# Optimization experiments

Hardware: AMD Instinct MI355X
Metric: run time of the kernel (lower is better)

Reference implementation:

```python
import jax, jax.numpy as jnp
import numpy as np

VOCAB = 50000
E = 300        # embedding_dim
HID = 512      # hidden_dim (bidirectional total)
HD = HID // 2  # per-direction hidden
K = 20         # tagset size
START = 18
STOP = 19
B = 64
T = 256
NEG = -10000.0


def setup_inputs() -> dict:
    key = jax.random.key(0)
    ks = jax.random.split(key, 12)
    s = 0.1
    sentence = jax.random.randint(ks[0], (B, T), 0, VOCAB)
    length = jax.random.randint(ks[1], (B,), T // 2, T + 1)
    embed_table = jax.random.normal(ks[2], (VOCAB, E)) * s
    w_ih_f = jax.random.normal(ks[3], (4 * HD, E)) * s
    w_hh_f = jax.random.normal(ks[4], (4 * HD, HD)) * s
    b_f = jax.random.normal(ks[5], (4 * HD,)) * s
    w_ih_b = jax.random.normal(ks[6], (4 * HD, E)) * s
    w_hh_b = jax.random.normal(ks[7], (4 * HD, HD)) * s
    b_b = jax.random.normal(ks[8], (4 * HD,)) * s
    W_out = jax.random.normal(ks[9], (K, HID)) * s
    b_out = jax.random.normal(ks[10], (K,)) * s
    transitions = jax.random.normal(ks[11], (K, K))
    transitions = transitions.at[START, :].set(NEG).at[:, STOP].set(NEG)
    return dict(sentence=sentence, length=length, embed_table=embed_table,
                w_ih_f=w_ih_f, w_hh_f=w_hh_f, b_f=b_f,
                w_ih_b=w_ih_b, w_hh_b=w_hh_b, b_b=b_b,
                W_out=W_out, b_out=b_out, transitions=transitions)


def _lstm(xs, w_ih, w_hh, b, reverse):
    # xs: [T, B, E]; PyTorch gate order i, f, g, o
    Bn = xs.shape[1]
    H = w_hh.shape[1]

    def step(carry, x):
        h, c = carry
        g = x @ w_ih.T + h @ w_hh.T + b
        i, f, gg, o = jnp.split(g, 4, axis=-1)
        c = jax.nn.sigmoid(f) * c + jax.nn.sigmoid(i) * jnp.tanh(gg)
        h = jax.nn.sigmoid(o) * jnp.tanh(c)
        return (h, c), h

    init = (jnp.zeros((Bn, H), xs.dtype), jnp.zeros((Bn, H), xs.dtype))
    _, hs = jax.lax.scan(step, init, xs, reverse=reverse)
    return hs  # [T, B, H], time-ordered


def _viterbi(feats, length, transitions):
    # feats: [B, T, K]; vectorized over batch, scan over time
    Bn, Tn, Kn = feats.shape
    fv0 = jnp.full((Bn, Kn), NEG, feats.dtype).at[:, START].set(0.0)
    idk = jnp.arange(Kn)

    def step(fv, inp):
        feat_t, t = inp
        # scores[b, next, prev] = fv[b, prev] + transitions[next, prev]
        sc = fv[:, None, :] + transitions[None, :, :]
        bp = jnp.argmax(sc, axis=-1)              # [B, K]
        best = jnp.max(sc, axis=-1) + feat_t      # [B, K]
        m = (t < length)[:, None]
        fv_new = jnp.where(m, best, fv)           # freeze past sentence end
        bp = jnp.where(m, bp, idk[None, :])       # identity backpointer on pad
        return fv_new, bp

    fv, bps = jax.lax.scan(step, fv0, (jnp.swapaxes(feats, 0, 1), jnp.arange(Tn)))
    term = fv + transitions[STOP][None, :]
    last = jnp.argmax(term, axis=-1)              # [B]
    score = jnp.max(term, axis=-1)                # [B] viterbi max score

    def back(tag, bp_t):
        prev = jnp.take_along_axis(bp_t, tag[:, None], axis=1)[:, 0]
        return prev, tag

    _, path_t = jax.lax.scan(back, last, bps, reverse=True)  # [T, B], time order
    path = jnp.swapaxes(path_t, 0, 1)             # [B, T]; entries >= length repeat last tag
    return score, path


def reference(sentence, length, embed_table, w_ih_f, w_hh_f, b_f,
              w_ih_b, w_hh_b, b_b, W_out, b_out, transitions):
    embeds = embed_table[sentence]                # [B, T, E]
    xs = jnp.swapaxes(embeds, 0, 1)               # [T, B, E]
    hf = _lstm(xs, w_ih_f, w_hh_f, b_f, reverse=False)
    hb = _lstm(xs, w_ih_b, w_hh_b, b_b, reverse=True)
    h = jnp.concatenate([hf, hb], axis=-1)        # [T, B, HID]
    feats = h @ W_out.T + b_out                   # [T, B, K]
    feats = jnp.swapaxes(feats, 0, 1)             # [B, T, K]
    score, path = _viterbi(feats, length, transitions)
    return score, path
```

## Files before the change

### kernel.cpp

```cpp
#include <hip/hip_runtime.h>
#include <hip/hip_bf16.h>

#define DINL __device__ __forceinline__

namespace {

typedef unsigned long long u64;

constexpr int Tn = 256;
constexpr int Bn = 64;
constexpr int HDn = 256;
constexpr int Kt = 20;
constexpr int STOPt = 19;
constexpr int STARTt = 18;
constexpr float NEGV = -10000.0f;

DINL float sigm(float x) { return 1.0f / (1.0f + __expf(-x)); }
DINL float tanh_f(float x) {
  float ax = fabsf(x);
  float e = __expf(-2.0f * ax);
  float t = (1.0f - e) / (1.0f + e);
  return x < 0.0f ? -t : t;
}

__global__ void k_epoch(unsigned* ep) {
  if (threadIdx.x == 0)
    __hip_atomic_fetch_add(ep, 1u, __ATOMIC_RELAXED, __HIP_MEMORY_SCOPE_AGENT);
}

__global__ void k_wt(const float* __restrict__ wf, const float* __restrict__ wb,
                     float* __restrict__ Wt) {
  int idx = blockIdx.x * 256 + threadIdx.x;
  if (idx >= 300 * 2048) return;
  int k = idx >> 11, n = idx & 2047;
  const float* w = (n < 1024) ? wf : wb;
  int nn = n & 1023;
  Wt[idx] = w[nn * 300 + k];
}

__global__ __launch_bounds__(256) void k_xproj(
    const int* __restrict__ sentence, const float* __restrict__ table,
    const float* __restrict__ Wt, const float* __restrict__ b_f,
    const float* __restrict__ b_b, float* __restrict__ xproj) {
  __shared__ float As[20][68];
  __shared__ float Bs[20][136];
  __shared__ int tok[64];

  int tid = threadIdx.x;
  int t = blockIdx.x;
  int n0 = blockIdx.y * 128;

  if (tid < 64) tok[tid] = sentence[tid * Tn + t];
  __syncthreads();

  int ty = tid >> 4, tx = tid & 15;
  float acc[4][8];
#pragma unroll
  for (int i = 0; i < 4; ++i)
#pragma unroll
    for (int j = 0; j < 8; ++j) acc[i][j] = 0.0f;

  for (int k0 = 0; k0 < 300; k0 += 20) {
#pragma unroll
    for (int i = 0; i < 5; ++i) {
      int idx = i * 256 + tid;
      int r = idx / 20, kk = idx % 20;
      As[kk][r] = table[tok[r] * 300 + k0 + kk];
    }
#pragma unroll
    for (int i = 0; i < 10; ++i) {
      int idx = i * 256 + tid;
      int kk = idx >> 7, c = idx & 127;
      Bs[kk][c] = Wt[(k0 + kk) * 2048 + n0 + c];
    }
    __syncthreads();
#pragma unroll
    for (int kk = 0; kk < 20; ++kk) {
      float4 a4 = *(const float4*)&As[kk][ty * 4];
      float4 b4a = *(const float4*)&Bs[kk][tx * 8];
      float4 b4b = *(const float4*)&Bs[kk][tx * 8 + 4];
      float av[4] = {a4.x, a4.y, a4.z, a4.w};
      float bvv[8] = {b4a.x, b4a.y, b4a.z, b4a.w, b4b.x, b4b.y, b4b.z, b4b.w};
#pragma unroll
      for (int i = 0; i < 4; ++i)
#pragma unroll
        for (int j = 0; j < 8; ++j) acc[i][j] += av[i] * bvv[j];
    }
    __syncthreads();
  }

  float bias[8];
#pragma unroll
  for (int j = 0; j < 8; ++j) {
    int n = n0 + tx * 8 + j;
    bias[j] = (n < 1024) ? b_f[n] : b_b[n - 1024];
  }
#pragma unroll
  for (int i = 0; i < 4; ++i) {
    size_t m = (size_t)t * 64 + ty * 4 + i;
    float* dst = &xproj[m * 2048 + n0 + tx * 8];
    float4 v0 = {acc[i][0] + bias[0], acc[i][1] + bias[1], acc[i][2] + bias[2],
                 acc[i][3] + bias[3]};
    float4 v1 = {acc[i][4] + bias[4], acc[i][5] + bias[5], acc[i][6] + bias[6],
                 acc[i][7] + bias[7]};
    *(float4*)dst = v0;
    *(float4*)(dst + 4) = v1;
  }
}

__global__ __launch_bounds__(128) void k_lstm(
    const float* __restrict__ whh_f, const float* __restrict__ whh_b,
    const float* __restrict__ xproj, float* __restrict__ h_all,
    int* __restrict__ flags, int* __restrict__ xcdtab,
    const unsigned* __restrict__ ep) {
  __shared__ __align__(16) float hl[16 * 256];
  __shared__ int fastsh;

  int tid = threadIdx.x;
  int bid = blockIdx.x;
  int gid = bid & 7;
  int s = bid >> 3;
  int dir = gid >> 2;
  int bg = gid & 3;
  const float* whh = dir ? whh_b : whh_f;

  int c = tid >> 4;
  int kc = tid & 15;

  unsigned E =
      __hip_atomic_load(ep, __ATOMIC_RELAXED, __HIP_MEMORY_SCOPE_AGENT);
  unsigned xcd = __builtin_amdgcn_s_getreg((3 << 11) | (0 << 6) | 20) & 0xFu;
  if (tid == 0) {
    __hip_atomic_store(&xcdtab[(gid << 5) + s],
                       (int)((E << 4) | xcd), __ATOMIC_RELAXED,
                       __HIP_MEMORY_SCOPE_AGENT);
  }
  if (tid < 64) {
    const int* xp_ = xcdtab + (gid << 5) + (tid & 31);
    unsigned v;
    for (;;) {
      v = (unsigned)__hip_atomic_load(xp_, __ATOMIC_RELAXED,
                                      __HIP_MEMORY_SCOPE_AGENT);
      bool rdy = (v >> 4) == (E & 0x0FFFFFFFu);
      if (__all((tid < 32) ? rdy : 1)) break;
      __builtin_amdgcn_s_sleep(1);
    }
    int mine = (int)(v & 0xFu);
    int ref = __shfl(mine, 0, 64);
    bool eq = (mine == ref);
    bool alleq = __all((tid < 32) ? eq : 1);
    if (tid == 0) fastsh = alleq ? 1 : 0;
  }

  float4 w4[4][4];
#pragma unroll
  for (int g = 0; g < 4; ++g) {
    const float* src = whh + ((size_t)(g * 256 + s * 8 + c)) * 256;
#pragma unroll
    for (int jj = 0; jj < 4; ++jj)
      w4[g][jj] = *(const float4*)(src + ((kc + (jj << 4)) << 2));
  }

  __syncthreads();
  const bool fast = (fastsh != 0);
  const unsigned base = E * 256u;

  float c_reg = 0.0f;

  for (int st = 0; st < Tn; ++st) {
    int xt = dir ? (Tn - 1 - st) : st;

    float xp[4];
    {
      size_t xb = ((size_t)(xt * 64 + bg * 16 + kc)) * 2048 + dir * 1024 +
                  s * 8 + c;
#pragma unroll
      for (int g = 0; g < 4; ++g) xp[g] = xproj[xb + g * 256];
    }

    float acc[16][4];
#pragma unroll
    for (int b = 0; b < 16; ++b)
#pragma unroll
      for (int g = 0; g < 4; ++g) acc[b][g] = 0.0f;

    if (st > 0) {
      if (tid < 64) {
        const int* fp = flags + ((gid << 5) + (tid & 31)) * 4;
        for (;;) {
          unsigned v = (unsigned)__hip_atomic_load(
              fp, __ATOMIC_RELAXED, __HIP_MEMORY_SCOPE_AGENT);
          int d = (int)(v - base);
          if (__all((tid < 32) ? (d >= st) : 1)) break;
          __builtin_amdgcn_s_sleep(1);
        }
      }
      __syncthreads();

      int pt = dir ? (xt + 1) : (xt - 1);
      const float* hsrc =
          h_all + ((size_t)(dir * Tn + pt) * 64 + bg * 16) * 256;
      const char* tb = (const char*)hsrc + (size_t)tid * 16;
      const char* p0 = tb;
      const char* p1 = tb + 4096;
      const char* p2 = tb + 8192;
      const char* p3 = tb + 12288;
      float4 q0, q1, q2, q3, q4, q5, q6, q7;
      asm volatile(
          "global_load_dwordx4 %0, %8, off sc1\n\t"
          "global_load_dwordx4 %1, %8, off offset:2048 sc1\n\t"
          "global_load_dwordx4 %2, %9, off sc1\n\t"
          "global_load_dwordx4 %3, %9, off offset:2048 sc1\n\t"
          "global_load_dwordx4 %4, %10, off sc1\n\t"
          "global_load_dwordx4 %5, %10, off offset:2048 sc1\n\t"
          "global_load_dwordx4 %6, %11, off sc1\n\t"
          "global_load_dwordx4 %7, %11, off offset:2048 sc1\n\t"
          "s_waitcnt vmcnt(0)"
          : "=&v"(q0), "=&v"(q1), "=&v"(q2), "=&v"(q3), "=&v"(q4), "=&v"(q5),
            "=&v"(q6), "=&v"(q7)
          : "v"(p0), "v"(p1), "v"(p2), "v"(p3));
      *(float4*)&hl[(tid + 0 * 128) << 2] = q0;
      *(float4*)&hl[(tid + 1 * 128) << 2] = q1;
      *(float4*)&hl[(tid + 2 * 128) << 2] = q2;
      *(float4*)&hl[(tid + 3 * 128) << 2] = q3;
      *(float4*)&hl[(tid + 4 * 128) << 2] = q4;
      *(float4*)&hl[(tid + 5 * 128) << 2] = q5;
      *(float4*)&hl[(tid + 6 * 128) << 2] = q6;
      *(float4*)&hl[(tid + 7 * 128) << 2] = q7;
      __syncthreads();

#pragma unroll
      for (int b = 0; b < 16; ++b) {
#pragma unroll
        for (int jj = 0; jj < 4; ++jj) {
          float4 hv = *(const float4*)&hl[b * 256 + ((kc + (jj << 4)) << 2)];
#pragma unroll
          for (int g = 0; g < 4; ++g) {
            acc[b][g] += w4[g][jj].x * hv.x + w4[g][jj].y * hv.y +
                         w4[g][jj].z * hv.z + w4[g][jj].w * hv.w;
          }
        }
      }
    }

#pragma unroll
    for (int r = 0; r < 4; ++r) {
      int m = 1 << r;
      int kb = (kc >> r) & 1;
#pragma unroll
      for (int ii = 0; ii < (16 >> (r + 1)); ++ii) {
#pragma unroll
        for (int g = 0; g < 4; ++g) {
          float e = acc[2 * ii][g], o = acc[2 * ii + 1][g];
          float kept = kb ? o : e;
          float sent = kb ? e : o;
          acc[ii][g] = kept + __shfl_xor(sent, m, 64);
        }
      }
    }

    {
      float gi = acc[0][0] + xp[0];
      float gf = acc[0][1] + xp[1];
      float gg = acc[0][2] + xp[2];
      float go = acc[0][3] + xp[3];
      c_reg = sigm(gf) * c_reg + sigm(gi) * tanh_f(gg);
      float h = sigm(go) * tanh_f(c_reg);
      size_t hi = ((size_t)(dir * Tn + xt) * 64 + bg * 16 + kc) * 256 + s * 8 +
                  c;
      if (fast) {
        h_all[hi] = h;
      } else {
        __hip_atomic_store(&h_all[hi], h, __ATOMIC_RELAXED,
                           __HIP_MEMORY_SCOPE_AGENT);
      }
    }

    asm volatile("s_waitcnt vmcnt(0)" ::: "memory");
    __syncthreads();
    if (tid == 0) {
      int fv = (int)(base + (unsigned)(st + 1));
      if (fast) {
        flags[((gid << 5) + s) * 4] = fv;
      } else {
        __hip_atomic_store(flags + ((gid << 5) + s) * 4, fv, __ATOMIC_RELAXED,
                           __HIP_MEMORY_SCOPE_AGENT);
      }
    }
  }
}

__global__ __launch_bounds__(256) void k_feats(const float* __restrict__ h_all,
                                               const float* __restrict__ Wout,
                                               const float* __restrict__ bout,
                                               float* __restrict__ feats) {
  __shared__ float Wl[20 * 512];
  __shared__ float hlf[64 * 256];

  int tid = threadIdx.x;
  int t = blockIdx.x;
  for (int i = tid; i < 20 * 512; i += 256) Wl[i] = Wout[i];

  float acc[5] = {0, 0, 0, 0, 0};
  int b = tid & 63, kg5 = tid >> 6;
  int swz = b & 7;

  for (int d = 0; d < 2; ++d) {
    __syncthreads();
    const float* hsrc = h_all + ((size_t)(d * Tn + t)) * 64 * 256;
#pragma unroll 8
    for (int i = 0; i < 64; ++i) {
      int idx = i * 256 + tid;
      int hb = idx >> 8, k = idx & 255;
      hlf[hb * 256 + 4 * ((k >> 2) ^ (hb & 7)) + (k & 3)] = hsrc[idx];
    }
    __syncthreads();
    for (int jg = 0; jg < 64; ++jg) {
      float4 hv = *(const float4*)&hlf[b * 256 + 4 * (jg ^ swz)];
#pragma unroll
      for (int kk = 0; kk < 5; ++kk) {
        int krow = kg5 * 5 + kk;
        float4 wvv = *(const float4*)&Wl[krow * 512 + d * 256 + jg * 4];
        acc[kk] += hv.x * wvv.x + hv.y * wvv.y + hv.z * wvv.z + hv.w * wvv.w;
      }
    }
  }
#pragma unroll
  for (int kk = 0; kk < 5; ++kk) {
    int krow = kg5 * 5 + kk;
    feats[((size_t)b * Tn + t) * Kt + krow] = acc[kk] + bout[krow];
  }
}

__global__ __launch_bounds__(64) void k_viterbi(const float* __restrict__ feats,
                                                const float* __restrict__ trans,
                                                const int* __restrict__ length,
                                                float* __restrict__ out) {
  __shared__ float tr[400];
  __shared__ float fv[20];
  __shared__ float term[20];
  __shared__ unsigned char bps[256][20];

  int b = blockIdx.x;
  int lane = threadIdx.x;
  for (int i = lane; i < 400; i += 64) tr[i] = trans[i];
  if (lane < 20) fv[lane] = (lane == STARTt) ? 0.0f : NEGV;
  int len = length[b];
  __syncthreads();

  for (int t = 0; t < Tn; ++t) {
    float nf = 0.0f;
    int bp = 0;
    if (lane < 20) {
      if (t < len) {
        float vmax = -3.4e38f;
        int pb = 0;
#pragma unroll
        for (int p = 0; p < 20; ++p) {
          float v = fv[p] + tr[lane * 20 + p];
          if (v > vmax) { vmax = v; pb = p; }
        }
        nf = vmax + feats[((size_t)b * Tn + t) * Kt + lane];
        bp = pb;
      } else {
        nf = fv[lane];
        bp = lane;
      }
    }
    __syncthreads();
    if (lane < 20) {
      fv[lane] = nf;
      bps[t][lane] = (unsigned char)bp;
    }
    __syncthreads();
  }

  if (lane < 20) term[lane] = fv[lane] + tr[STOPt * 20 + lane];
  __syncthreads();
  if (lane == 0) {
    float smax = term[0];
    int last = 0;
    for (int p = 1; p < 20; ++p)
      if (term[p] > smax) { smax = term[p]; last = p; }
    out[b] = smax;
    int tag = last;
    for (int t = Tn - 1; t >= 0; --t) {
      out[64 + b * Tn + t] = (float)tag;
      tag = bps[t][tag];
    }
  }
}

}

extern "C" void kernel_launch(void* const* d_in, const int* in_sizes, int n_in,
                              void* d_out, int out_size, void* d_ws,
                              size_t ws_size, hipStream_t stream) {
  const int* sentence = (const int*)d_in[0];
  const int* length = (const int*)d_in[1];
  const float* table = (const float*)d_in[2];
  const float* w_ih_f = (const float*)d_in[3];
  const float* w_hh_f = (const float*)d_in[4];
  const float* b_f = (const float*)d_in[5];
  const float* w_ih_b = (const float*)d_in[6];
  const float* w_hh_b = (const float*)d_in[7];
  const float* b_b = (const float*)d_in[8];
  const float* W_out = (const float*)d_in[9];
  const float* b_out = (const float*)d_in[10];
  const float* trans = (const float*)d_in[11];
  float* out = (float*)d_out;

  float* ws = (float*)d_ws;
  float* xproj = ws;
  float* h_all = ws + (size_t)33554432;
  float* Wt = h_all + (size_t)8388608;
  float* feats = Wt + (size_t)300 * 2048;
  int* flags = (int*)(feats + (size_t)Bn * Tn * Kt);
  int* xcdtab = flags + 1024;
  unsigned* ep = (unsigned*)(xcdtab + 256);
  (void)ws_size; (void)in_sizes; (void)n_in; (void)out_size;

  k_epoch<<<dim3(1), dim3(64), 0, stream>>>(ep);
  k_wt<<<dim3(2400), dim3(256), 0, stream>>>(w_ih_f, w_ih_b, Wt);
  k_xproj<<<dim3(256, 16), dim3(256), 0, stream>>>(sentence, table, Wt, b_f,
                                                   b_b, xproj);
  k_lstm<<<dim3(256), dim3(128), 0, stream>>>(w_hh_f, w_hh_b, xproj, h_all,
                                              flags, xcdtab, ep);
  k_feats<<<dim3(256), dim3(256), 0, stream>>>(h_all, W_out, b_out, feats);
  k_viterbi<<<dim3(64), dim3(64), 0, stream>>>(feats, trans, length, out);
}
```

Baseline: 1.480 ms.

## Replace LSTM per-step flag barrier with epoch-tagged hidden-state words

Each hidden value is now stored as a 64-bit word that packs the float with an epoch-and-step tag. Consumers check these tags directly instead of polling a separate per-block flag array after a store-drain and block barrier, which takes the flag round-trip and the producer-side waitcnt/syncthreads off the sequential recurrence. The cost is twice the bytes per hidden-state read and write, plus a retry loop that re-reads the whole batch when tags are stale. The xproj loads also become nontemporal.

```diff
diff --git a/kernel.cpp b/kernel.cpp
--- a/kernel.cpp
+++ b/kernel.cpp
@@ -21,6 +21,10 @@
   float e = __expf(-2.0f * ax);
   float t = (1.0f - e) / (1.0f + e);
   return x < 0.0f ? -t : t;
+}
+
+DINL void agent_st64(u64* p, u64 v) {
+  __hip_atomic_store(p, v, __ATOMIC_RELAXED, __HIP_MEMORY_SCOPE_AGENT);
 }
 
 __global__ void k_epoch(unsigned* ep) {
@@ -110,9 +114,8 @@
 
 __global__ __launch_bounds__(128) void k_lstm(
     const float* __restrict__ whh_f, const float* __restrict__ whh_b,
-    const float* __restrict__ xproj, float* __restrict__ h_all,
-    int* __restrict__ flags, int* __restrict__ xcdtab,
-    const unsigned* __restrict__ ep) {
+    const float* __restrict__ xproj, u64* __restrict__ h_ep,
+    int* __restrict__ xcdtab, const unsigned* __restrict__ ep) {
   __shared__ __align__(16) float hl[16 * 256];
   __shared__ int fastsh;
 
@@ -131,9 +134,8 @@
       __hip_atomic_load(ep, __ATOMIC_RELAXED, __HIP_MEMORY_SCOPE_AGENT);
   unsigned xcd = __builtin_amdgcn_s_getreg((3 << 11) | (0 << 6) | 20) & 0xFu;
   if (tid == 0) {
-    __hip_atomic_store(&xcdtab[(gid << 5) + s],
-                       (int)((E << 4) | xcd), __ATOMIC_RELAXED,
-                       __HIP_MEMORY_SCOPE_AGENT);
+    __hip_atomic_store(&xcdtab[(gid << 5) + s], (int)((E << 4) | xcd),
+                       __ATOMIC_RELAXED, __HIP_MEMORY_SCOPE_AGENT);
   }
   if (tid < 64) {
     const int* xp_ = xcdtab + (gid << 5) + (tid & 31);
@@ -163,7 +165,7 @@
 
   __syncthreads();
   const bool fast = (fastsh != 0);
-  const unsigned base = E * 256u;
+  const unsigned base = E * 512u;
 
   float c_reg = 0.0f;
 
@@ -175,7 +177,8 @@
       size_t xb = ((size_t)(xt * 64 + bg * 16 + kc)) * 2048 + dir * 1024 +
                   s * 8 + c;
 #pragma unroll
-      for (int g = 0; g < 4; ++g) xp[g] = xproj[xb + g * 256];
+      for (int g = 0; g < 4; ++g)
+        xp[g] = __builtin_nontemporal_load(&xproj[xb + g * 256]);
     }
 
     float acc[16][4];
@@ -185,48 +188,83 @@
       for (int g = 0; g < 4; ++g) acc[b][g] = 0.0f;
 
     if (st > 0) {
-      if (tid < 64) {
-        const int* fp = flags + ((gid << 5) + (tid & 31)) * 4;
-        for (;;) {
-          unsigned v = (unsigned)__hip_atomic_load(
-              fp, __ATOMIC_RELAXED, __HIP_MEMORY_SCOPE_AGENT);
-          int d = (int)(v - base);
-          if (__all((tid < 32) ? (d >= st) : 1)) break;
-          __builtin_amdgcn_s_sleep(1);
-        }
-      }
-      __syncthreads();
-
       int pt = dir ? (xt + 1) : (xt - 1);
-      const float* hsrc =
-          h_all + ((size_t)(dir * Tn + pt) * 64 + bg * 16) * 256;
+      const u64* hsrc =
+          h_ep + ((size_t)(dir * Tn + pt) * 64 + bg * 16) * 256;
       const char* tb = (const char*)hsrc + (size_t)tid * 16;
       const char* p0 = tb;
       const char* p1 = tb + 4096;
       const char* p2 = tb + 8192;
       const char* p3 = tb + 12288;
-      float4 q0, q1, q2, q3, q4, q5, q6, q7;
-      asm volatile(
-          "global_load_dwordx4 %0, %8, off sc1\n\t"
-          "global_load_dwordx4 %1, %8, off offset:2048 sc1\n\t"
-          "global_load_dwordx4 %2, %9, off sc1\n\t"
-          "global_load_dwordx4 %3, %9, off offset:2048 sc1\n\t"
-          "global_load_dwordx4 %4, %10, off sc1\n\t"
-          "global_load_dwordx4 %5, %10, off offset:2048 sc1\n\t"
-          "global_load_dwordx4 %6, %11, off sc1\n\t"
-          "global_load_dwordx4 %7, %11, off offset:2048 sc1\n\t"
-          "s_waitcnt vmcnt(0)"
-          : "=&v"(q0), "=&v"(q1), "=&v"(q2), "=&v"(q3), "=&v"(q4), "=&v"(q5),
-            "=&v"(q6), "=&v"(q7)
-          : "v"(p0), "v"(p1), "v"(p2), "v"(p3));
-      *(float4*)&hl[(tid + 0 * 128) << 2] = q0;
-      *(float4*)&hl[(tid + 1 * 128) << 2] = q1;
-      *(float4*)&hl[(tid + 2 * 128) << 2] = q2;
-      *(float4*)&hl[(tid + 3 * 128) << 2] = q3;
-      *(float4*)&hl[(tid + 4 * 128) << 2] = q4;
-      *(float4*)&hl[(tid + 5 * 128) << 2] = q5;
-      *(float4*)&hl[(tid + 6 * 128) << 2] = q6;
-      *(float4*)&hl[(tid + 7 * 128) << 2] = q7;
+      const char* p4 = tb + 16384;
+      const char* p5 = tb + 20480;
+      const char* p6 = tb + 24576;
+      const char* p7 = tb + 28672;
+      uint4 q0, q1, q2, q3, q4, q5, q6, q7;
+      uint4 q8, q9, q10, q11, q12, q13, q14, q15;
+      unsigned tgt = base + (unsigned)st;
+#define BATCH_READ()                                                        \
+  asm volatile(                                                             \
+      "global_load_dwordx4 %0, %16, off sc1\n\t"                            \
+      "global_load_dwordx4 %1, %16, off offset:2048 sc1\n\t"                \
+      "global_load_dwordx4 %2, %17, off sc1\n\t"                            \
+      "global_load_dwordx4 %3, %17, off offset:2048 sc1\n\t"                \
+      "global_load_dwordx4 %4, %18, off sc1\n\t"                            \
+      "global_load_dwordx4 %5, %18, off offset:2048 sc1\n\t"                \
+      "global_load_dwordx4 %6, %19, off sc1\n\t"                            \
+      "global_load_dwordx4 %7, %19, off offset:2048 sc1\n\t"                \
+      "global_load_dwordx4 %8, %20, off sc1\n\t"                            \
+      "global_load_dwordx4 %9, %20, off offset:2048 sc1\n\t"                \
+      "global_load_dwordx4 %10, %21, off sc1\n\t"                           \
+      "global_load_dwordx4 %11, %21, off offset:2048 sc1\n\t"               \
+      "global_load_dwordx4 %12, %22, off sc1\n\t"                           \
+      "global_load_dwordx4 %13, %22, off offset:2048 sc1\n\t"               \
+      "global_load_dwordx4 %14, %23, off sc1\n\t"                           \
+      "global_load_dwordx4 %15, %23, off offset:2048 sc1\n\t"               \
+      "s_waitcnt vmcnt(0)"                                                  \
+      : "=&v"(q0), "=&v"(q1), "=&v"(q2), "=&v"(q3), "=&v"(q4), "=&v"(q5),   \
+        "=&v"(q6), "=&v"(q7), "=&v"(q8), "=&v"(q9), "=&v"(q10), "=&v"(q11), \
+        "=&v"(q12), "=&v"(q13), "=&v"(q14), "=&v"(q15)                      \
+      : "v"(p0), "v"(p1), "v"(p2), "v"(p3), "v"(p4), "v"(p5), "v"(p6),      \
+        "v"(p7))
+#define TAGS_OK()                                                            \
+  ((q0.y == tgt) & (q0.w == tgt) & (q1.y == tgt) & (q1.w == tgt) &           \
+   (q2.y == tgt) & (q2.w == tgt) & (q3.y == tgt) & (q3.w == tgt) &           \
+   (q4.y == tgt) & (q4.w == tgt) & (q5.y == tgt) & (q5.w == tgt) &           \
+   (q6.y == tgt) & (q6.w == tgt) & (q7.y == tgt) & (q7.w == tgt) &           \
+   (q8.y == tgt) & (q8.w == tgt) & (q9.y == tgt) & (q9.w == tgt) &           \
+   (q10.y == tgt) & (q10.w == tgt) & (q11.y == tgt) & (q11.w == tgt) &       \
+   (q12.y == tgt) & (q12.w == tgt) & (q13.y == tgt) & (q13.w == tgt) &       \
+   (q14.y == tgt) & (q14.w == tgt) & (q15.y == tgt) & (q15.w == tgt))
+      BATCH_READ();
+      while (!TAGS_OK()) {
+        for (;;) {
+          unsigned v;
+          asm volatile(
+              "global_load_dword %0, %1, off offset:2052 sc1\n\t"
+              "s_waitcnt vmcnt(0)"
+              : "=v"(v)
+              : "v"(p7));
+          if (v == tgt) break;
+          __builtin_amdgcn_s_sleep(1);
+        }
+        BATCH_READ();
+      }
+#undef BATCH_READ
+#undef TAGS_OK
+      __syncthreads();
+#define STAGE(Q, I)                                          \
+  {                                                          \
+    float2 fv_;                                              \
+    fv_.x = __uint_as_float((Q).x);                          \
+    fv_.y = __uint_as_float((Q).z);                          \
+    *(float2*)&hl[((I) << 8) + (tid << 1)] = fv_;            \
+  }
+      STAGE(q0, 0)  STAGE(q1, 1)  STAGE(q2, 2)  STAGE(q3, 3)
+      STAGE(q4, 4)  STAGE(q5, 5)  STAGE(q6, 6)  STAGE(q7, 7)
+      STAGE(q8, 8)  STAGE(q9, 9)  STAGE(q10, 10) STAGE(q11, 11)
+      STAGE(q12, 12) STAGE(q13, 13) STAGE(q14, 14) STAGE(q15, 15)
+#undef STAGE
       __syncthreads();
 
 #pragma unroll
@@ -266,31 +304,20 @@
       float go = acc[0][3] + xp[3];
       c_reg = sigm(gf) * c_reg + sigm(gi) * tanh_f(gg);
       float h = sigm(go) * tanh_f(c_reg);
-      size_t hi = ((size_t)(dir * Tn + xt) * 64 + bg * 16 + kc) * 256 + s * 8 +
-                  c;
+      u64 pk = ((u64)(base + (unsigned)(st + 1)) << 32) |
+               (u64)__float_as_uint(h);
+      u64* dst = &h_ep[((size_t)(dir * Tn + xt) * 64 + bg * 16 + kc) * 256 +
+                       s * 8 + c];
       if (fast) {
-        h_all[hi] = h;
+        *dst = pk;
       } else {
-        __hip_atomic_store(&h_all[hi], h, __ATOMIC_RELAXED,
-                           __HIP_MEMORY_SCOPE_AGENT);
-      }
-    }
-
-    asm volatile("s_waitcnt vmcnt(0)" ::: "memory");
-    __syncthreads();
-    if (tid == 0) {
-      int fv = (int)(base + (unsigned)(st + 1));
-      if (fast) {
-        flags[((gid << 5) + s) * 4] = fv;
-      } else {
-        __hip_atomic_store(flags + ((gid << 5) + s) * 4, fv, __ATOMIC_RELAXED,
-                           __HIP_MEMORY_SCOPE_AGENT);
-      }
-    }
-  }
-}
-
-__global__ __launch_bounds__(256) void k_feats(const float* __restrict__ h_all,
+        agent_st64(dst, pk);
+      }
+    }
+  }
+}
+
+__global__ __launch_bounds__(256) void k_feats(const u64* __restrict__ h_ep,
                                                const float* __restrict__ Wout,
                                                const float* __restrict__ bout,
                                                float* __restrict__ feats) {
@@ -307,12 +334,14 @@
 
   for (int d = 0; d < 2; ++d) {
     __syncthreads();
-    const float* hsrc = h_all + ((size_t)(d * Tn + t)) * 64 * 256;
+    const u64* hsrc = h_ep + ((size_t)(d * Tn + t)) * 64 * 256;
 #pragma unroll 8
     for (int i = 0; i < 64; ++i) {
       int idx = i * 256 + tid;
       int hb = idx >> 8, k = idx & 255;
-      hlf[hb * 256 + 4 * ((k >> 2) ^ (hb & 7)) + (k & 3)] = hsrc[idx];
+      u64 pk = hsrc[idx];
+      hlf[hb * 256 + 4 * ((k >> 2) ^ (hb & 7)) + (k & 3)] =
+          __uint_as_float((unsigned)pk);
     }
     __syncthreads();
     for (int jg = 0; jg < 64; ++jg) {
@@ -412,11 +441,10 @@
 
   float* ws = (float*)d_ws;
   float* xproj = ws;
-  float* h_all = ws + (size_t)33554432;
-  float* Wt = h_all + (size_t)8388608;
+  u64* h_ep = (u64*)(ws + (size_t)33554432);
+  float* Wt = ws + (size_t)33554432 + 16777216;
   float* feats = Wt + (size_t)300 * 2048;
-  int* flags = (int*)(feats + (size_t)Bn * Tn * Kt);
-  int* xcdtab = flags + 1024;
+  int* xcdtab = (int*)(feats + (size_t)Bn * Tn * Kt);
   unsigned* ep = (unsigned*)(xcdtab + 256);
   (void)ws_size; (void)in_sizes; (void)n_in; (void)out_size;
 
@@ -424,8 +452,8 @@
   k_wt<<<dim3(2400), dim3(256), 0, stream>>>(w_ih_f, w_ih_b, Wt);
   k_xproj<<<dim3(256, 16), dim3(256), 0, stream>>>(sentence, table, Wt, b_f,
                                                    b_b, xproj);
-  k_lstm<<<dim3(256), dim3(128), 0, stream>>>(w_hh_f, w_hh_b, xproj, h_all,
-                                              flags, xcdtab, ep);
-  k_feats<<<dim3(256), dim3(256), 0, stream>>>(h_all, W_out, b_out, feats);
+  k_lstm<<<dim3(256), dim3(128), 0, stream>>>(w_hh_f, w_hh_b, xproj, h_ep,
+                                              xcdtab, ep);
+  k_feats<<<dim3(256), dim3(256), 0, stream>>>(h_ep, W_out, b_out, feats);
   k_viterbi<<<dim3(64), dim3(64), 0, stream>>>(feats, trans, length, out);
 }
```

After: 1.705 ms. 1.15x slower.
